# Kernel optimization log

Hardware: AMD Instinct MI355X
Metric: run time of the kernel (lower is better)

Reference implementation:

```python
import jax, jax.numpy as jnp
import numpy as np

E = 768       # embedding_dim
H = 12        # num_heads
ID = 768      # inter_dim
HD = ID // H  # head_dim = 64
DHX = HD // 2  # 32
DHY = HD - DHX  # 32
HP, WP = 16, 16
P = HP * WP
BASE = 10000.0
SCALE = HD ** -0.5


def rot_half(x):
    x1 = x[..., 0::2]
    x2 = x[..., 1::2]
    return jnp.stack([-x2, x1], axis=-1).reshape(x.shape)


def apply_rope(x, cos, sin):
    cos = jnp.repeat(cos, 2, axis=-1)
    sin = jnp.repeat(sin, 2, axis=-1)
    return x * cos + rot_half(x) * sin


def rope_cache(L, dim, base):
    inv_freq = 1.0 / base ** (jnp.arange(0, dim, 2, dtype=jnp.float32) / dim)
    t = jnp.arange(L, dtype=jnp.float32)
    freqs = t[:, None] * inv_freq[None, :]  # [L, dim//2]
    return jnp.cos(freqs), jnp.sin(freqs)


def _rope_tables():
    yy, xx = jnp.meshgrid(jnp.arange(HP), jnp.arange(WP), indexing='ij')
    py = yy.reshape(P)
    px = xx.reshape(P)
    cos_x, sin_x = rope_cache(WP, DHX, BASE)
    cos_y, sin_y = rope_cache(HP, DHY, BASE)
    # gather per-patch tables, shape (1,1,P,1,D/2)
    cx = cos_x[px].reshape(1, 1, P, 1, DHX // 2)
    sx = sin_x[px].reshape(1, 1, P, 1, DHX // 2)
    cy = cos_y[py].reshape(1, 1, P, 1, DHY // 2)
    sy = sin_y[py].reshape(1, 1, P, 1, DHY // 2)
    return cx, sx, cy, sy


def setup_inputs() -> dict:
    key = jax.random.key(0)
    ks = jax.random.split(key, 8)
    B, T = 8, 16
    x = jax.random.normal(ks[0], (B, T, P, E), dtype=jnp.float32)
    s = 0.02
    return {
        'x': x,
        'Wq': jax.random.normal(ks[1], (E, ID), dtype=jnp.float32) * s,
        'bq': jnp.zeros((ID,), dtype=jnp.float32),
        'Wk': jax.random.normal(ks[2], (E, ID), dtype=jnp.float32) * s,
        'bk': jnp.zeros((ID,), dtype=jnp.float32),
        'Wv': jax.random.normal(ks[3], (E, ID), dtype=jnp.float32) * s,
        'bv': jnp.zeros((ID,), dtype=jnp.float32),
        'Wo': jax.random.normal(ks[4], (ID, E), dtype=jnp.float32) * s,
    }


def reference(x, Wq, bq, Wk, bk, Wv, bv, Wo):
    B, T, Pn, _ = x.shape
    q = (x @ Wq + bq).reshape(B, T, Pn, H, HD)
    k = (x @ Wk + bk).reshape(B, T, Pn, H, HD)
    v = (x @ Wv + bv).reshape(B, T, Pn, H, HD)

    cx, sx, cy, sy = _rope_tables()
    qx, qy = q[..., :DHX], q[..., DHX:]
    kx, ky = k[..., :DHX], k[..., DHX:]
    q = jnp.concatenate([apply_rope(qx, cx, sx), apply_rope(qy, cy, sy)], axis=-1)
    k = jnp.concatenate([apply_rope(kx, cx, sx), apply_rope(ky, cy, sy)], axis=-1)

    scores = jnp.einsum('btihd,btjhd->bthij', q, k) * SCALE
    probs = jax.nn.softmax(scores, axis=-1)
    y = jnp.einsum('bthij,btjhd->btihd', probs, v).reshape(B, T, Pn, ID)
    return y @ Wo
```

## Files before the change

### kernel.cpp

```cpp
#include <hip/hip_runtime.h>
#include <hip/hip_bf16.h>
#include <cstdint>
#include <cstddef>

typedef __bf16 bf16;
typedef __bf16 bf16x8 __attribute__((ext_vector_type(8)));
typedef __bf16 bf16x4 __attribute__((ext_vector_type(4)));
typedef float  f32x4  __attribute__((ext_vector_type(4)));

#define MFMA_BF16(a,b,c) __builtin_amdgcn_mfma_f32_16x16x32_bf16((a),(b),(c),0,0,0)

#define BB 8
#define TT 16
#define PP 256
#define EE 768
#define HH 12
#define HDD 64
#define NQKV 2304
#define MROWS 32768

__device__ __forceinline__ void gld_lds16(const bf16* g, bf16* l) {
  __builtin_amdgcn_global_load_lds((const __attribute__((address_space(1))) void*)g,
                                   (__attribute__((address_space(3))) void*)l, 16, 0, 0);
}

__global__ __launch_bounds__(256) void k_cvt_x(const float* __restrict__ x,
                                               bf16* __restrict__ xb) {
  const int64_t i = (int64_t)blockIdx.x * 256 + threadIdx.x;
  const float4* src = (const float4*)x;
  float4 a = src[i * 2];
  float4 b = src[i * 2 + 1];
  bf16x8 o;
  o[0] = (bf16)a.x; o[1] = (bf16)a.y; o[2] = (bf16)a.z; o[3] = (bf16)a.w;
  o[4] = (bf16)b.x; o[5] = (bf16)b.y; o[6] = (bf16)b.z; o[7] = (bf16)b.w;
  *(bf16x8*)(xb + i * 8) = o;
}

__global__ __launch_bounds__(256) void k_wt(const float* __restrict__ Wq,
                                            const float* __restrict__ Wk,
                                            const float* __restrict__ Wv,
                                            const float* __restrict__ Wo,
                                            bf16* __restrict__ wt) {
  __shared__ float tile[32][33];
  const int n0 = blockIdx.x * 32;
  const int k0 = blockIdx.y * 32;
  const float* W;
  int nc;
  if (n0 < 768)        { W = Wq; nc = n0; }
  else if (n0 < 1536)  { W = Wk; nc = n0 - 768; }
  else if (n0 < 2304)  { W = Wv; nc = n0 - 1536; }
  else                 { W = Wo; nc = n0 - 2304; }
  const int tx = threadIdx.x & 31, ty = threadIdx.x >> 5;
  for (int r = ty; r < 32; r += 8)
    tile[r][tx] = W[(int64_t)(k0 + r) * 768 + nc + tx];
  __syncthreads();
  for (int r = ty; r < 32; r += 8)
    wt[(int64_t)(n0 + r) * 768 + k0 + tx] = (bf16)tile[tx][r];
}

__global__ __launch_bounds__(512, 2) void k_qkv(const bf16* __restrict__ xb,
                                                const bf16* __restrict__ wt,
                                                const float* __restrict__ bq,
                                                const float* __restrict__ bk,
                                                const float* __restrict__ bv,
                                                bf16* __restrict__ qb,
                                                bf16* __restrict__ kb,
                                                bf16* __restrict__ vt) {
  extern __shared__ char smem_raw[];
  bf16* smem = (bf16*)smem_raw;
  const int tid = threadIdx.x;
  const int w = tid >> 6, lane = tid & 63, quad = lane >> 4, l16 = lane & 15;
  const int wr = w >> 2, wc = w & 3;
  const int kap = l16 & 7;
  const int bid = blockIdx.x;
  const int xcd = bid & 7;
  const int loc = bid >> 3;
  const int m0  = (xcd * 16 + loc / 9) * 256;
  const int n0  = (loc % 9) * 256;
  const int srow = w * 8 + (lane >> 3);
  const int cgo  = ((lane & 7) ^ ((lane >> 3) & 7)) * 8;
  const bf16* Ag = xb + (int64_t)(m0 + srow) * 768 + cgo;
  const bf16* Bg = wt + (int64_t)(n0 + srow) * 768 + cgo;

  auto stage = [&](int kt, int p) {
    bf16* LA = smem + p * 32768 + w * 512;
    bf16* LB = LA + 16384;
    const bf16* GA = Ag + kt * 64;
    const bf16* GB = Bg + kt * 64;
#pragma unroll
    for (int rd = 0; rd < 4; ++rd) {
      gld_lds16(GA + rd * 49152, LA + rd * 4096);
      gld_lds16(GB + rd * 49152, LB + rd * 4096);
    }
  };

  f32x4 acc[8][4] = {};
  stage(0, 0);
  __syncthreads();
  for (int t = 0; t < 12; ++t) {
    if (t < 11) stage(t + 1, (t + 1) & 1);
    __builtin_amdgcn_sched_barrier(0);
    const bf16* A = smem + (t & 1) * 32768;
    const bf16* B = A + 16384;
    bf16x8 bfr[4][2];
#pragma unroll
    for (int ni = 0; ni < 4; ++ni)
#pragma unroll
      for (int kk = 0; kk < 2; ++kk)
        bfr[ni][kk] = *(const bf16x8*)&B[(wc * 64 + ni * 16 + l16) * 64 +
                                         (((kk * 4 + quad) ^ kap) * 8)];
#pragma unroll
    for (int mh = 0; mh < 2; ++mh) {
      bf16x8 afr[4][2];
#pragma unroll
      for (int mi = 0; mi < 4; ++mi)
#pragma unroll
        for (int kk = 0; kk < 2; ++kk)
          afr[mi][kk] = *(const bf16x8*)&A[(wr * 128 + mh * 64 + mi * 16 + l16) * 64 +
                                           (((kk * 4 + quad) ^ kap) * 8)];
      __builtin_amdgcn_s_setprio(1);
#pragma unroll
      for (int mi = 0; mi < 4; ++mi)
#pragma unroll
        for (int ni = 0; ni < 4; ++ni)
#pragma unroll
          for (int kk = 0; kk < 2; ++kk)
            acc[mh * 4 + mi][ni] = MFMA_BF16(afr[mi][kk], bfr[ni][kk], acc[mh * 4 + mi][ni]);
      __builtin_amdgcn_s_setprio(0);
    }
    __syncthreads();
  }
  const int sec = n0 / 768;
  const int h0 = (n0 % 768) >> 6;
  const float* bias_p = (sec == 0) ? bq : (sec == 1) ? bk : bv;
  char* eb = (char*)smem;
  const int64_t obase = (int64_t)(m0 >> 8) * 12 * 16384;
  if (sec == 2) {
#pragma unroll
    for (int ni = 0; ni < 4; ++ni) {
      const int nn = wc * 64 + ni * 16 + l16;
      const int hh = nn >> 6, hd = nn & 63;
      const float bias = bias_p[(n0 % 768) + nn];
#pragma unroll
      for (int mi = 0; mi < 8; ++mi) {
        const int p = wr * 128 + mi * 16 + quad * 4;
        bf16x4 pk;
#pragma unroll
        for (int r = 0; r < 4; ++r) pk[r] = (bf16)(acc[mi][ni][r] + bias);
        *(bf16x4*)(eb + hh * 32768 + hd * 512 +
                   ((((p >> 3) ^ (hd & 15)) << 4) | (((p >> 2) & 1) << 3))) = pk;
      }
    }
    __syncthreads();
#pragma unroll
    for (int it = 0; it < 16; ++it) {
      const int lin = (it * 512 + tid) * 16;
      const int hh = lin >> 15;
      const int rem = lin & 32767;
      const int hd = rem >> 9;
      const int cs = (rem >> 4) & 31;
      const int pc = cs ^ (hd & 15);
      bf16x8 val = *(const bf16x8*)(eb + lin);
      *(bf16x8*)&vt[obase + ((int64_t)(h0 + hh) * 64 + hd) * 256 + pc * 8] = val;
    }
  } else {
    bf16* dst = (sec == 0) ? qb : kb;
    const float L2C = 0.83048202372184058696f;
#pragma unroll
    for (int ni = 0; ni < 4; ++ni) {
      const int nn = wc * 64 + ni * 16 + l16;
      const int hh = nn >> 6, hd = nn & 63;
      const float bias = bias_p[(n0 % 768) + nn];
      const int j = (hd & 31) >> 1;
      const float invf = exp2f(-(float)j * L2C);
      const bool odd = (hd & 1);
      const bool isx = (hd < 32);
      float snt[8], cst[8];
      if (isx) {
#pragma unroll
        for (int r = 0; r < 4; ++r)
          __sincosf((float)(quad * 4 + r) * invf, &snt[r], &cst[r]);
      } else {
#pragma unroll
        for (int mi = 0; mi < 8; ++mi)
          __sincosf((float)(wr * 8 + mi) * invf, &snt[mi], &cst[mi]);
      }
#pragma unroll
      for (int mi = 0; mi < 8; ++mi) {
#pragma unroll
        for (int r = 0; r < 4; ++r) {
          const int p = wr * 128 + mi * 16 + quad * 4 + r;
          float v = acc[mi][ni][r] + bias;
          float pv = __shfl_xor(v, 1, 64);
          const float sn = isx ? snt[r] : snt[mi];
          const float cz = isx ? cst[r] : cst[mi];
          float o = odd ? (v * cz + pv * sn) : (v * cz - pv * sn);
          *(bf16*)(eb + hh * 32768 + p * 128 +
                   ((((hd >> 3) ^ (p & 7)) << 4) | ((hd & 7) << 1))) = (bf16)o;
        }
      }
    }
    __syncthreads();
#pragma unroll
    for (int it = 0; it < 16; ++it) {
      const int lin = (it * 512 + tid) * 16;
      const int hh = lin >> 15;
      const int rem = lin & 32767;
      const int p = rem >> 7;
      const int cs = (rem >> 4) & 7;
      const int hc = cs ^ (p & 7);
      bf16x8 val = *(const bf16x8*)(eb + lin);
      *(bf16x8*)&dst[obase + ((int64_t)(h0 + hh) * 256 + p) * 64 + hc * 8] = val;
    }
  }
}

__global__ __launch_bounds__(256) void k_attn(bf16* qy,
                                              const bf16* __restrict__ kb,
                                              const bf16* __restrict__ vt) {
  __shared__ __align__(16) bf16 plds[4][16 * 264];
  const int tid = threadIdx.x;
  const int w = tid >> 6, lane = tid & 63, quad = lane >> 4, l16 = lane & 15;
  const int64_t base = (int64_t)blockIdx.x * 16384;
  bf16* Q = qy + base;
  const bf16* K = kb + base;
  const bf16* V = vt + base;
  bf16* pl = plds[w];
  for (int s = 0; s < 4; ++s) {
    const int r0 = w * 64 + s * 16;
    bf16x8 qf0 = *(const bf16x8*)&Q[(r0 + l16) * 64 + quad * 8];
    bf16x8 qf1 = *(const bf16x8*)&Q[(r0 + l16) * 64 + 32 + quad * 8];
    f32x4 sacc[16] = {};
    __builtin_amdgcn_s_setprio(1);
#pragma unroll
    for (int ct = 0; ct < 16; ++ct) {
      bf16x8 kf0 = *(const bf16x8*)&K[(ct * 16 + l16) * 64 + quad * 8];
      bf16x8 kf1 = *(const bf16x8*)&K[(ct * 16 + l16) * 64 + 32 + quad * 8];
      sacc[ct] = MFMA_BF16(qf0, kf0, sacc[ct]);
      sacc[ct] = MFMA_BF16(qf1, kf1, sacc[ct]);
    }
    __builtin_amdgcn_s_setprio(0);
    float mx[4] = {-3e38f, -3e38f, -3e38f, -3e38f};
#pragma unroll
    for (int ct = 0; ct < 16; ++ct)
#pragma unroll
      for (int r = 0; r < 4; ++r) mx[r] = fmaxf(mx[r], sacc[ct][r]);
#pragma unroll
    for (int d = 1; d < 16; d <<= 1)
#pragma unroll
      for (int r = 0; r < 4; ++r) mx[r] = fmaxf(mx[r], __shfl_xor(mx[r], d, 64));
    float sm[4] = {0.f, 0.f, 0.f, 0.f};
#pragma unroll
    for (int ct = 0; ct < 16; ++ct)
#pragma unroll
      for (int r = 0; r < 4; ++r) {
        float e = __expf((sacc[ct][r] - mx[r]) * 0.125f);
        sacc[ct][r] = e;
        sm[r] += e;
      }
#pragma unroll
    for (int d = 1; d < 16; d <<= 1)
#pragma unroll
      for (int r = 0; r < 4; ++r) sm[r] += __shfl_xor(sm[r], d, 64);
#pragma unroll
    for (int ct = 0; ct < 16; ++ct)
#pragma unroll
      for (int r = 0; r < 4; ++r)
        pl[(quad * 4 + r) * 264 + ct * 16 + l16] = (bf16)sacc[ct][r];
    asm volatile("s_waitcnt lgkmcnt(0)" ::: "memory");
    __builtin_amdgcn_sched_barrier(0);
    f32x4 oacc[4] = {};
    __builtin_amdgcn_s_setprio(1);
#pragma unroll
    for (int kc = 0; kc < 8; ++kc) {
      bf16x8 pf = *(const bf16x8*)&pl[l16 * 264 + kc * 32 + quad * 8];
#pragma unroll
      for (int nt = 0; nt < 4; ++nt) {
        bf16x8 vf = *(const bf16x8*)&V[(nt * 16 + l16) * 256 + kc * 32 + quad * 8];
        oacc[nt] = MFMA_BF16(pf, vf, oacc[nt]);
      }
    }
    __builtin_amdgcn_s_setprio(0);
    float inv[4];
#pragma unroll
    for (int r = 0; r < 4; ++r) inv[r] = 1.0f / sm[r];
#pragma unroll
    for (int nt = 0; nt < 4; ++nt)
#pragma unroll
      for (int r = 0; r < 4; ++r)
        Q[(r0 + quad * 4 + r) * 64 + nt * 16 + l16] = (bf16)(oacc[nt][r] * inv[r]);
    asm volatile("" ::: "memory");
  }
}

__global__ __launch_bounds__(512, 2) void k_out(const bf16* __restrict__ yb,
                                                const bf16* __restrict__ wt,
                                                float* __restrict__ out) {
  extern __shared__ char smem_raw[];
  bf16* smem = (bf16*)smem_raw;
  const int tid = threadIdx.x;
  const int w = tid >> 6, lane = tid & 63, quad = lane >> 4, l16 = lane & 15;
  const int wr = w >> 1, wc = w & 1;
  const int bid = blockIdx.x;
  const int xcd = bid & 7;
  const int loc = bid >> 3;
  const int m0  = (xcd * 16 + loc / 6) * 256;
  const int n0  = (loc % 6) * 128;
  const int bt  = m0 >> 8;
  const int srow = w * 8 + (lane >> 3);
  const int cgo  = (((lane & 7) ^ ((lane >> 3) & 7)) * 8);
  const bf16* Bg0 = wt + (int64_t)(2304 + n0 + srow) * 768 + cgo;

  auto stage = [&](int kt, int p) {
    bf16* LA = smem + p * 24576 + w * 512;
    bf16* LB = smem + p * 24576 + 16384 + w * 512;
    const bf16* GA = yb + (int64_t)(bt * 12 + kt) * 16384 + srow * 64 + cgo;
    const bf16* GB = Bg0 + kt * 64;
#pragma unroll
    for (int rd = 0; rd < 4; ++rd)
      gld_lds16(GA + rd * 4096, LA + rd * 4096);
#pragma unroll
    for (int rd = 0; rd < 2; ++rd)
      gld_lds16(GB + rd * 49152, LB + rd * 4096);
  };

  f32x4 acc[4][4] = {};
  stage(0, 0);
  __syncthreads();
  const int rkey8 = (l16 & 7) * 8;
  for (int t = 0; t < 12; ++t) {
    if (t < 11) stage(t + 1, (t + 1) & 1);
    __builtin_amdgcn_sched_barrier(0);
    const bf16* A = smem + (t & 1) * 24576;
    const bf16* B = A + 16384;
    bf16x8 bfr[4][2];
#pragma unroll
    for (int ni = 0; ni < 4; ++ni)
#pragma unroll
      for (int kk = 0; kk < 2; ++kk)
        bfr[ni][kk] = *(const bf16x8*)&B[(wc * 64 + ni * 16 + l16) * 64 +
                                         (((kk * 4 + quad) * 8) ^ rkey8)];
    bf16x8 afr[4][2];
#pragma unroll
    for (int mi = 0; mi < 4; ++mi)
#pragma unroll
      for (int kk = 0; kk < 2; ++kk)
        afr[mi][kk] = *(const bf16x8*)&A[(wr * 64 + mi * 16 + l16) * 64 +
                                         (((kk * 4 + quad) * 8) ^ rkey8)];
    __builtin_amdgcn_s_setprio(1);
#pragma unroll
    for (int mi = 0; mi < 4; ++mi)
#pragma unroll
      for (int ni = 0; ni < 4; ++ni)
#pragma unroll
        for (int kk = 0; kk < 2; ++kk)
          acc[mi][ni] = MFMA_BF16(afr[mi][kk], bfr[ni][kk], acc[mi][ni]);
    __builtin_amdgcn_s_setprio(0);
    __syncthreads();
  }
#pragma unroll
  for (int mi = 0; mi < 4; ++mi)
#pragma unroll
    for (int ni = 0; ni < 4; ++ni) {
      const int rg = m0 + wr * 64 + mi * 16 + quad * 4;
      const int cg = n0 + wc * 64 + ni * 16 + l16;
#pragma unroll
      for (int r = 0; r < 4; ++r)
        out[(int64_t)(rg + r) * 768 + cg] = acc[mi][ni][r];
    }
}

extern "C" void kernel_launch(void* const* d_in, const int* in_sizes, int n_in,
                              void* d_out, int out_size, void* d_ws, size_t ws_size,
                              hipStream_t stream) {
  const float* x  = (const float*)d_in[0];
  const float* Wq = (const float*)d_in[1];
  const float* bq = (const float*)d_in[2];
  const float* Wk = (const float*)d_in[3];
  const float* bk = (const float*)d_in[4];
  const float* Wv = (const float*)d_in[5];
  const float* bv = (const float*)d_in[6];
  const float* Wo = (const float*)d_in[7];
  float* out = (float*)d_out;

  uint8_t* ws = (uint8_t*)d_ws;
  const size_t SZ = (size_t)25165824 * 2;
  bf16* qy = (bf16*)ws;
  bf16* kb = (bf16*)(ws + SZ);
  bf16* vt = (bf16*)(ws + 2 * SZ);
  bf16* wt = (bf16*)(ws + 3 * SZ);
  bf16* xb = (bf16*)d_out;

  static int attr_set = 0;
  if (!attr_set) {
    (void)hipFuncSetAttribute((const void*)k_qkv,
                              hipFuncAttributeMaxDynamicSharedMemorySize, 131072);
    (void)hipFuncSetAttribute((const void*)k_out,
                              hipFuncAttributeMaxDynamicSharedMemorySize, 98304);
    attr_set = 1;
  }

  k_cvt_x<<<12288, 256, 0, stream>>>(x, xb);
  k_wt<<<dim3(96, 24), 256, 0, stream>>>(Wq, Wk, Wv, Wo, wt);
  k_qkv<<<1152, 512, 131072, stream>>>(xb, wt, bq, bk, bv, qy, kb, vt);
  k_attn<<<1536, 256, 0, stream>>>(qy, kb, vt);
  k_out<<<768, 512, 98304, stream>>>(qy, wt, out);
}
```

Baseline: 533.7 us.

## Stage K and V tiles in swizzled LDS for attention with 512-thread blocks

The attention kernel now copies each (b,t,h) block's K and V tiles into LDS with direct global-to-LDS loads and an XOR swizzle. MFMA operands are then read from LDS instead of global memory. Blocks grow to 512 threads (8 waves, 32 query rows each), so the staged K/V is shared by more waves. The cost is about 130 KB of dynamic LDS per block, which limits occupancy, plus a barrier before compute with no overlap between the load and the math.

After: 452.5 us. 15.2% less time.

```diff
diff --git a/kernel.cpp b/kernel.cpp
--- a/kernel.cpp
+++ b/kernel.cpp
@@ -215,27 +215,42 @@
   }
 }
 
-__global__ __launch_bounds__(256) void k_attn(bf16* qy,
-                                              const bf16* __restrict__ kb,
-                                              const bf16* __restrict__ vt) {
-  __shared__ __align__(16) bf16 plds[4][16 * 264];
+__global__ __launch_bounds__(512, 2) void k_attn(bf16* qy,
+                                                 const bf16* __restrict__ kb,
+                                                 const bf16* __restrict__ vt) {
+  extern __shared__ char smem_raw[];
+  bf16* lK = (bf16*)smem_raw;
+  bf16* lV = lK + 16384;
+  bf16* plds = lV + 16384;
   const int tid = threadIdx.x;
   const int w = tid >> 6, lane = tid & 63, quad = lane >> 4, l16 = lane & 15;
   const int64_t base = (int64_t)blockIdx.x * 16384;
   bf16* Q = qy + base;
   const bf16* K = kb + base;
   const bf16* V = vt + base;
-  bf16* pl = plds[w];
-  for (int s = 0; s < 4; ++s) {
-    const int r0 = w * 64 + s * 16;
+  bf16* pl = plds + w * 4224;
+#pragma unroll
+  for (int rd = 0; rd < 4; ++rd) {
+    const int ci = rd * 512 + tid;
+    const int krow = ci >> 3, kch = ci & 7;
+    gld_lds16(K + krow * 64 + ((kch ^ (krow & 7)) << 3),
+              lK + (rd * 512 + w * 64) * 8);
+    const int vrow = ci >> 5, vch = ci & 31;
+    gld_lds16(V + vrow * 256 + ((vch ^ (vrow & 7)) << 3),
+              lV + (rd * 512 + w * 64) * 8);
+  }
+  __syncthreads();
+  for (int s = 0; s < 2; ++s) {
+    const int r0 = w * 32 + s * 16;
     bf16x8 qf0 = *(const bf16x8*)&Q[(r0 + l16) * 64 + quad * 8];
     bf16x8 qf1 = *(const bf16x8*)&Q[(r0 + l16) * 64 + 32 + quad * 8];
     f32x4 sacc[16] = {};
     __builtin_amdgcn_s_setprio(1);
 #pragma unroll
     for (int ct = 0; ct < 16; ++ct) {
-      bf16x8 kf0 = *(const bf16x8*)&K[(ct * 16 + l16) * 64 + quad * 8];
-      bf16x8 kf1 = *(const bf16x8*)&K[(ct * 16 + l16) * 64 + 32 + quad * 8];
+      const int kr = ct * 16 + l16;
+      bf16x8 kf0 = *(const bf16x8*)&lK[kr * 64 + ((quad ^ (kr & 7)) << 3)];
+      bf16x8 kf1 = *(const bf16x8*)&lK[kr * 64 + (((quad + 4) ^ (kr & 7)) << 3)];
       sacc[ct] = MFMA_BF16(qf0, kf0, sacc[ct]);
       sacc[ct] = MFMA_BF16(qf1, kf1, sacc[ct]);
     }
@@ -276,7 +291,8 @@
       bf16x8 pf = *(const bf16x8*)&pl[l16 * 264 + kc * 32 + quad * 8];
 #pragma unroll
       for (int nt = 0; nt < 4; ++nt) {
-        bf16x8 vf = *(const bf16x8*)&V[(nt * 16 + l16) * 256 + kc * 32 + quad * 8];
+        const int vr = nt * 16 + l16;
+        bf16x8 vf = *(const bf16x8*)&lV[vr * 256 + (((kc * 4 + quad) ^ (vr & 7)) << 3)];
         oacc[nt] = MFMA_BF16(pf, vf, oacc[nt]);
       }
     }
@@ -395,6 +411,8 @@
   if (!attr_set) {
     (void)hipFuncSetAttribute((const void*)k_qkv,
                               hipFuncAttributeMaxDynamicSharedMemorySize, 131072);
+    (void)hipFuncSetAttribute((const void*)k_attn,
+                              hipFuncAttributeMaxDynamicSharedMemorySize, 133120);
     (void)hipFuncSetAttribute((const void*)k_out,
                               hipFuncAttributeMaxDynamicSharedMemorySize, 98304);
     attr_set = 1;
@@ -403,6 +421,6 @@
   k_cvt_x<<<12288, 256, 0, stream>>>(x, xb);
   k_wt<<<dim3(96, 24), 256, 0, stream>>>(Wq, Wk, Wv, Wo, wt);
   k_qkv<<<1152, 512, 131072, stream>>>(xb, wt, bq, bk, bv, qy, kb, vt);
-  k_attn<<<1536, 256, 0, stream>>>(qy, kb, vt);
+  k_attn<<<1536, 512, 133120, stream>>>(qy, kb, vt);
   k_out<<<768, 512, 98304, stream>>>(qy, wt, out);
 }
```
